# Optimization experiments

Measured on AMD Instinct MI355X. Metric: run time of the kernel, lower is better.

## Reference

```python
import jax, jax.numpy as jnp
import numpy as np

N_NODES = 50000
N_EDGES = 800000
D = 128


def setup_inputs() -> dict:
    key = jax.random.key(0)
    ks = jax.random.split(key, 8)
    scale = 1.0 / np.sqrt(D)
    x = jax.random.normal(ks[0], (N_NODES, D), dtype=jnp.float32)
    edge_index = jax.random.randint(ks[1], (2, N_EDGES), 0, N_NODES, dtype=jnp.int64)
    return {
        "x": x,
        "edge_index": edge_index,
        "w1_l": jax.random.normal(ks[2], (D, D), dtype=jnp.float32) * scale,
        "w1_r": jax.random.normal(ks[3], (D, D), dtype=jnp.float32) * scale,
        "b1": jnp.zeros((D,), dtype=jnp.float32),
        "w2_l": jax.random.normal(ks[4], (D, D), dtype=jnp.float32) * scale,
        "w2_r": jax.random.normal(ks[5], (D, D), dtype=jnp.float32) * scale,
        "b2": jnp.zeros((D,), dtype=jnp.float32),
    }


def _sage_conv(x, src, dst, w_l, w_r, b):
    # mean aggregation of source features at destination nodes
    n = x.shape[0]
    msg = x[src]                                            # [E, D] gather
    agg = jax.ops.segment_sum(msg, dst, num_segments=n)      # [N, D] scatter-add
    cnt = jax.ops.segment_sum(jnp.ones((src.shape[0],), x.dtype), dst, num_segments=n)
    mean = agg / jnp.maximum(cnt, 1.0)[:, None]
    # out = lin_l(mean_agg) + lin_r(x) + bias  (PyG SAGEConv default)
    return mean @ w_l.T + x @ w_r.T + b


def reference(x, edge_index, w1_l, w1_r, b1, w2_l, w2_r, b2):
    src, dst = edge_index[0], edge_index[1]
    h = jax.nn.relu(_sage_conv(x, src, dst, w1_l, w1_r, b1))
    out = _sage_conv(h, src, dst, w2_l, w2_r, b2)
    return out
```

## Files before the change

kernel.cpp:

```cpp
#include <hip/hip_runtime.h>

#define D 128
#define CAP 48
#define TILE 16

typedef unsigned short u16;
typedef unsigned int u32;
typedef _Float16 f16;
typedef __attribute__((ext_vector_type(4))) _Float16 h4;
typedef __attribute__((ext_vector_type(8))) _Float16 h8;
typedef __attribute__((ext_vector_type(4))) float f32x4;

__global__ __launch_bounds__(256) void prep_kernel(const float* __restrict__ x,
                                                   f16* __restrict__ xh, int n8,
                                                   const float* __restrict__ w1l,
                                                   const float* __restrict__ w1r,
                                                   const float* __restrict__ w2l,
                                                   const float* __restrict__ w2r,
                                                   f16* __restrict__ wb1,
                                                   f16* __restrict__ wb2,
                                                   int* __restrict__ cnt, int Nceil,
                                                   int cvtBlocks, int wBlocks) {
    const int b = blockIdx.x;
    const int t = threadIdx.x;
    if (b < cvtBlocks) {
        int i = b * 256 + t;
        if (i < n8) {
            float4 v0 = reinterpret_cast<const float4*>(x)[2 * i];
            float4 v1 = reinterpret_cast<const float4*>(x)[2 * i + 1];
            h8 o;
            o[0] = (f16)v0.x; o[1] = (f16)v0.y; o[2] = (f16)v0.z; o[3] = (f16)v0.w;
            o[4] = (f16)v1.x; o[5] = (f16)v1.y; o[6] = (f16)v1.z; o[7] = (f16)v1.w;
            reinterpret_cast<h8*>(xh)[i] = o;
        }
    } else if (b < cvtBlocks + wBlocks) {
        int e = (b - cvtBlocks) * 256 + t;
        int which = e >> 15;
        int i = e & 32767;
        int j = i >> 8, k = i & 255;
        const float* wl = which ? w2l : w1l;
        const float* wr = which ? w2r : w1r;
        f16* wb = which ? wb2 : wb1;
        float v = (k < 128) ? wl[j * 128 + k] : wr[j * 128 + k - 128];
        wb[i] = (f16)v;
    } else {
        int i = (b - cvtBlocks - wBlocks) * 256 + t;
        if (i < Nceil) cnt[i] = 0;
    }
}

__global__ __launch_bounds__(256) void fill_pad_xcd(const int* __restrict__ src,
                                                    const int* __restrict__ dst,
                                                    int* __restrict__ cnt,
                                                    int* __restrict__ edge_pad,
                                                    int E, int bucketDiv, int perChunk) {
    const int b = blockIdx.x & 7;
    const int chunk = blockIdx.x >> 3;
    const int lo = b * bucketDiv;
    const int hi = lo + bucketDiv;
    const int beg = chunk * perChunk;
    const int end = min(E, beg + perChunk);
    for (int base = beg + threadIdx.x * 4; base < end; base += 1024) {
        if (base + 3 < end) {
            int4 d = *reinterpret_cast<const int4*>(dst + base);
            if (d.x >= lo && d.x < hi) { int p = atomicAdd(&cnt[d.x], 1); if (p < CAP) edge_pad[d.x * CAP + p] = src[base + 0]; }
            if (d.y >= lo && d.y < hi) { int p = atomicAdd(&cnt[d.y], 1); if (p < CAP) edge_pad[d.y * CAP + p] = src[base + 1]; }
            if (d.z >= lo && d.z < hi) { int p = atomicAdd(&cnt[d.z], 1); if (p < CAP) edge_pad[d.z * CAP + p] = src[base + 2]; }
            if (d.w >= lo && d.w < hi) { int p = atomicAdd(&cnt[d.w], 1); if (p < CAP) edge_pad[d.w * CAP + p] = src[base + 3]; }
        } else {
            for (int j = 0; j < 4 && base + j < end; ++j) {
                int d = dst[base + j];
                if (d >= lo && d < hi) { int p = atomicAdd(&cnt[d], 1); if (p < CAP) edge_pad[d * CAP + p] = src[base + j]; }
            }
        }
    }
}

template <int RELU, int OUTF16>
__global__ __launch_bounds__(256) void sage_fused(const f16* __restrict__ feat,
                                                  const int* __restrict__ cnt,
                                                  const int* __restrict__ edge_pad,
                                                  const f16* __restrict__ wb,
                                                  const float* __restrict__ bias,
                                                  float* __restrict__ outf,
                                                  f16* __restrict__ outh, int n) {
    __shared__ f16 sM[TILE * 128];
    __shared__ int eLds[TILE * CAP];
    __shared__ int degLds[TILE];
    const int t = threadIdx.x;
    const int base = blockIdx.x * TILE;
    char* sMb = reinterpret_cast<char*>(sM);

    {
        const int4* gseg = reinterpret_cast<const int4*>(edge_pad + (size_t)base * CAP);
        if (t < TILE * CAP / 4) reinterpret_cast<int4*>(eLds)[t] = gseg[t];
        if (t < TILE) degLds[t] = (base + t < n) ? cnt[base + t] : 0;
    }
    __syncthreads();

    {
        const int halfId = t >> 5;
        const int lane = t & 31;
#pragma unroll
        for (int rnd = 0; rnd < TILE / 8; ++rnd) {
            const int nl = rnd * 8 + halfId;
            const int deg = degLds[nl];
            const int stored = min(deg, CAP);
            const int* ep = &eLds[nl * CAP];

            h4 acc = (h4){0, 0, 0, 0};
            int j = 0;
            for (; j + 16 <= stored; j += 16) {
                int4 i0 = *reinterpret_cast<const int4*>(ep + j);
                int4 i1 = *reinterpret_cast<const int4*>(ep + j + 4);
                int4 i2 = *reinterpret_cast<const int4*>(ep + j + 8);
                int4 i3 = *reinterpret_cast<const int4*>(ep + j + 12);
                h4 v0 = *reinterpret_cast<const h4*>(feat + (size_t)i0.x * D + lane * 4);
                h4 v1 = *reinterpret_cast<const h4*>(feat + (size_t)i0.y * D + lane * 4);
                h4 v2 = *reinterpret_cast<const h4*>(feat + (size_t)i0.z * D + lane * 4);
                h4 v3 = *reinterpret_cast<const h4*>(feat + (size_t)i0.w * D + lane * 4);
                h4 v4 = *reinterpret_cast<const h4*>(feat + (size_t)i1.x * D + lane * 4);
                h4 v5 = *reinterpret_cast<const h4*>(feat + (size_t)i1.y * D + lane * 4);
                h4 v6 = *reinterpret_cast<const h4*>(feat + (size_t)i1.z * D + lane * 4);
                h4 v7 = *reinterpret_cast<const h4*>(feat + (size_t)i1.w * D + lane * 4);
                h4 v8 = *reinterpret_cast<const h4*>(feat + (size_t)i2.x * D + lane * 4);
                h4 v9 = *reinterpret_cast<const h4*>(feat + (size_t)i2.y * D + lane * 4);
                h4 va = *reinterpret_cast<const h4*>(feat + (size_t)i2.z * D + lane * 4);
                h4 vb = *reinterpret_cast<const h4*>(feat + (size_t)i2.w * D + lane * 4);
                h4 vc = *reinterpret_cast<const h4*>(feat + (size_t)i3.x * D + lane * 4);
                h4 vd = *reinterpret_cast<const h4*>(feat + (size_t)i3.y * D + lane * 4);
                h4 ve = *reinterpret_cast<const h4*>(feat + (size_t)i3.z * D + lane * 4);
                h4 vf = *reinterpret_cast<const h4*>(feat + (size_t)i3.w * D + lane * 4);
                acc += ((v0 + v1) + (v2 + v3)) + ((v4 + v5) + (v6 + v7))
                     + ((v8 + v9) + (va + vb)) + ((vc + vd) + (ve + vf));
            }
            for (; j + 4 <= stored; j += 4) {
                int4 ia = *reinterpret_cast<const int4*>(ep + j);
                h4 v0 = *reinterpret_cast<const h4*>(feat + (size_t)ia.x * D + lane * 4);
                h4 v1 = *reinterpret_cast<const h4*>(feat + (size_t)ia.y * D + lane * 4);
                h4 v2 = *reinterpret_cast<const h4*>(feat + (size_t)ia.z * D + lane * 4);
                h4 v3 = *reinterpret_cast<const h4*>(feat + (size_t)ia.w * D + lane * 4);
                acc += (v0 + v1) + (v2 + v3);
            }
            for (; j < stored; ++j) {
                int s = ep[j];
                acc += *reinterpret_cast<const h4*>(feat + (size_t)s * D + lane * 4);
            }

            const f16 sc = (deg > 0) ? (f16)(1.f / (float)deg) : (f16)0;
            h4 o = acc * (h4){sc, sc, sc, sc};
            int lin = nl * 256 + lane * 8;
            *reinterpret_cast<h4*>(sMb + (lin ^ ((nl & 7) << 4))) = o;
        }
    }
    __syncthreads();

    const int wid = t >> 6, lane = t & 63;
    const int l15 = lane & 15, l4 = lane >> 4;
    const int colBase = wid * 32;

    int rowA = base + l15;
    if (rowA >= n) rowA = 0;

    f32x4 acc0 = (f32x4){0.f, 0.f, 0.f, 0.f};
    f32x4 acc1 = (f32x4){0.f, 0.f, 0.f, 0.f};

    const int swr = (l15 & 7) << 4;

#pragma unroll
    for (int ks = 0; ks < 8; ++ks) {
        h8 afr;
        if (ks < 4) {
            int lin = l15 * 256 + ks * 64 + l4 * 16;
            afr = *reinterpret_cast<const h8*>(sMb + (lin ^ swr));
        } else {
            const int kk = (ks & 3) * 32 + l4 * 8;
            afr = *reinterpret_cast<const h8*>(feat + (size_t)rowA * D + kk);
        }
#pragma unroll
        for (int q = 0; q < 2; ++q) {
            h8 bfr = *reinterpret_cast<const h8*>(
                wb + (size_t)(colBase + q * 16 + l15) * 256 + ks * 32 + l4 * 8);
            f32x4& a = q ? acc1 : acc0;
            a = __builtin_amdgcn_mfma_f32_16x16x32_f16(afr, bfr, a, 0, 0, 0);
        }
    }

#pragma unroll
    for (int q = 0; q < 2; ++q) {
        const int col = colBase + q * 16 + l15;
        const float bv = bias[col];
        const f32x4& a = q ? acc1 : acc0;
#pragma unroll
        for (int r = 0; r < 4; ++r) {
            int orow = base + l4 * 4 + r;
            if (orow < n) {
                float v = a[r] + bv;
                if (RELU) v = fmaxf(v, 0.f);
                if (OUTF16)
                    outh[(size_t)orow * D + col] = (f16)v;
                else
                    outf[(size_t)orow * D + col] = v;
            }
        }
    }
}

extern "C" void kernel_launch(void* const* d_in, const int* in_sizes, int n_in,
                              void* d_out, int out_size, void* d_ws, size_t ws_size,
                              hipStream_t stream) {
    const float* x   = (const float*)d_in[0];
    const int*   ei  = (const int*)d_in[1];
    const float* w1l = (const float*)d_in[2];
    const float* w1r = (const float*)d_in[3];
    const float* b1  = (const float*)d_in[4];
    const float* w2l = (const float*)d_in[5];
    const float* w2r = (const float*)d_in[6];
    const float* b2  = (const float*)d_in[7];
    float* out = (float*)d_out;

    const int N = in_sizes[0] / D;
    const int E = in_sizes[1] / 2;

    const int* src = ei;
    const int* dst = ei + E;

    const int gridFused = (N + TILE - 1) / TILE;
    const int Nceil = gridFused * TILE;

    char* ws = (char*)d_ws;
    auto align = [](size_t v) { return (v + 255) & ~(size_t)255; };
    const size_t featB = align((size_t)N * D * sizeof(f16));

    f16* xh       = (f16*)ws;   ws += featB;
    f16* hh       = (f16*)ws;   ws += featB;
    f16* wb1      = (f16*)ws;   ws += align(128 * 256 * sizeof(f16));
    f16* wb2      = (f16*)ws;   ws += align(128 * 256 * sizeof(f16));
    int* cnt      = (int*)ws;   ws += align((size_t)Nceil * sizeof(int));
    int* edge_pad = (int*)ws;   ws += align((size_t)Nceil * CAP * sizeof(int));

    const int n8        = N * D / 8;
    const int cvtBlocks = (n8 + 255) / 256;
    const int wBlocks   = 256;
    const int zBlocks   = (Nceil + 255) / 256;
    const int bucketDiv = (N + 7) / 8;
    const int perChunk  = 5120;
    const int chunks    = (E + perChunk - 1) / perChunk;

    prep_kernel<<<cvtBlocks + wBlocks + zBlocks, 256, 0, stream>>>(
        x, xh, n8, w1l, w1r, w2l, w2r, wb1, wb2, cnt, Nceil, cvtBlocks, wBlocks);

    fill_pad_xcd<<<8 * chunks, 256, 0, stream>>>(src, dst, cnt, edge_pad, E, bucketDiv, perChunk);

    sage_fused<1, 1><<<gridFused, 256, 0, stream>>>(xh, cnt, edge_pad, wb1, b1, nullptr, hh, N);

    sage_fused<0, 0><<<gridFused, 256, 0, stream>>>(hh, cnt, edge_pad, wb2, b2, out, nullptr, N);
}
```

Baseline: 170.3 us.

## Merge edge bucketing into prep kernel and double fused tile rows

```diff
diff --git a/kernel.cpp b/kernel.cpp
--- a/kernel.cpp
+++ b/kernel.cpp
@@ -2,7 +2,7 @@
 
 #define D 128
 #define CAP 48
-#define TILE 16
+#define TILE 32
 
 typedef unsigned short u16;
 typedef unsigned int u32;
@@ -11,16 +11,20 @@
 typedef __attribute__((ext_vector_type(8))) _Float16 h8;
 typedef __attribute__((ext_vector_type(4))) float f32x4;
 
-__global__ __launch_bounds__(256) void prep_kernel(const float* __restrict__ x,
-                                                   f16* __restrict__ xh, int n8,
-                                                   const float* __restrict__ w1l,
-                                                   const float* __restrict__ w1r,
-                                                   const float* __restrict__ w2l,
-                                                   const float* __restrict__ w2r,
-                                                   f16* __restrict__ wb1,
-                                                   f16* __restrict__ wb2,
-                                                   int* __restrict__ cnt, int Nceil,
-                                                   int cvtBlocks, int wBlocks) {
+__global__ __launch_bounds__(256) void mega_prep(const float* __restrict__ x,
+                                                 f16* __restrict__ xh, int n8,
+                                                 const float* __restrict__ w1l,
+                                                 const float* __restrict__ w1r,
+                                                 const float* __restrict__ w2l,
+                                                 const float* __restrict__ w2r,
+                                                 f16* __restrict__ wb1,
+                                                 f16* __restrict__ wb2,
+                                                 const int* __restrict__ src,
+                                                 const int* __restrict__ dst,
+                                                 int* __restrict__ cnt,
+                                                 int* __restrict__ edge_pad,
+                                                 int E, int bucketDiv, int perChunk,
+                                                 int cvtBlocks, int wBlocks) {
     const int b = blockIdx.x;
     const int t = threadIdx.x;
     if (b < cvtBlocks) {
@@ -44,33 +48,25 @@
         float v = (k < 128) ? wl[j * 128 + k] : wr[j * 128 + k - 128];
         wb[i] = (f16)v;
     } else {
-        int i = (b - cvtBlocks - wBlocks) * 256 + t;
-        if (i < Nceil) cnt[i] = 0;
-    }
-}
-
-__global__ __launch_bounds__(256) void fill_pad_xcd(const int* __restrict__ src,
-                                                    const int* __restrict__ dst,
-                                                    int* __restrict__ cnt,
-                                                    int* __restrict__ edge_pad,
-                                                    int E, int bucketDiv, int perChunk) {
-    const int b = blockIdx.x & 7;
-    const int chunk = blockIdx.x >> 3;
-    const int lo = b * bucketDiv;
-    const int hi = lo + bucketDiv;
-    const int beg = chunk * perChunk;
-    const int end = min(E, beg + perChunk);
-    for (int base = beg + threadIdx.x * 4; base < end; base += 1024) {
-        if (base + 3 < end) {
-            int4 d = *reinterpret_cast<const int4*>(dst + base);
-            if (d.x >= lo && d.x < hi) { int p = atomicAdd(&cnt[d.x], 1); if (p < CAP) edge_pad[d.x * CAP + p] = src[base + 0]; }
-            if (d.y >= lo && d.y < hi) { int p = atomicAdd(&cnt[d.y], 1); if (p < CAP) edge_pad[d.y * CAP + p] = src[base + 1]; }
-            if (d.z >= lo && d.z < hi) { int p = atomicAdd(&cnt[d.z], 1); if (p < CAP) edge_pad[d.z * CAP + p] = src[base + 2]; }
-            if (d.w >= lo && d.w < hi) { int p = atomicAdd(&cnt[d.w], 1); if (p < CAP) edge_pad[d.w * CAP + p] = src[base + 3]; }
-        } else {
-            for (int j = 0; j < 4 && base + j < end; ++j) {
-                int d = dst[base + j];
-                if (d >= lo && d < hi) { int p = atomicAdd(&cnt[d], 1); if (p < CAP) edge_pad[d * CAP + p] = src[base + j]; }
+        const int fillIdx = b - cvtBlocks - wBlocks;
+        const int bucket = b & 7;
+        const int chunk = fillIdx >> 3;
+        const int lo = bucket * bucketDiv;
+        const int hi = lo + bucketDiv;
+        const int beg = chunk * perChunk;
+        const int end = min(E, beg + perChunk);
+        for (int base = beg + t * 4; base < end; base += 1024) {
+            if (base + 3 < end) {
+                int4 d = *reinterpret_cast<const int4*>(dst + base);
+                if (d.x >= lo && d.x < hi) { int p = atomicAdd(&cnt[d.x], 1); if (p < CAP) edge_pad[d.x * CAP + p] = src[base + 0]; }
+                if (d.y >= lo && d.y < hi) { int p = atomicAdd(&cnt[d.y], 1); if (p < CAP) edge_pad[d.y * CAP + p] = src[base + 1]; }
+                if (d.z >= lo && d.z < hi) { int p = atomicAdd(&cnt[d.z], 1); if (p < CAP) edge_pad[d.z * CAP + p] = src[base + 2]; }
+                if (d.w >= lo && d.w < hi) { int p = atomicAdd(&cnt[d.w], 1); if (p < CAP) edge_pad[d.w * CAP + p] = src[base + 3]; }
+            } else {
+                for (int j = 0; j < 4 && base + j < end; ++j) {
+                    int d = dst[base + j];
+                    if (d >= lo && d < hi) { int p = atomicAdd(&cnt[d], 1); if (p < CAP) edge_pad[d * CAP + p] = src[base + j]; }
+                }
             }
         }
     }
@@ -93,7 +89,11 @@
 
     {
         const int4* gseg = reinterpret_cast<const int4*>(edge_pad + (size_t)base * CAP);
-        if (t < TILE * CAP / 4) reinterpret_cast<int4*>(eLds)[t] = gseg[t];
+#pragma unroll
+        for (int i = 0; i < (TILE * CAP / 4 + 255) / 256; ++i) {
+            int idx = i * 256 + t;
+            if (idx < TILE * CAP / 4) reinterpret_cast<int4*>(eLds)[idx] = gseg[idx];
+        }
         if (t < TILE) degLds[t] = (base + t < n) ? cnt[base + t] : 0;
     }
     __syncthreads();
@@ -110,29 +110,18 @@
 
             h4 acc = (h4){0, 0, 0, 0};
             int j = 0;
-            for (; j + 16 <= stored; j += 16) {
-                int4 i0 = *reinterpret_cast<const int4*>(ep + j);
-                int4 i1 = *reinterpret_cast<const int4*>(ep + j + 4);
-                int4 i2 = *reinterpret_cast<const int4*>(ep + j + 8);
-                int4 i3 = *reinterpret_cast<const int4*>(ep + j + 12);
-                h4 v0 = *reinterpret_cast<const h4*>(feat + (size_t)i0.x * D + lane * 4);
-                h4 v1 = *reinterpret_cast<const h4*>(feat + (size_t)i0.y * D + lane * 4);
-                h4 v2 = *reinterpret_cast<const h4*>(feat + (size_t)i0.z * D + lane * 4);
-                h4 v3 = *reinterpret_cast<const h4*>(feat + (size_t)i0.w * D + lane * 4);
-                h4 v4 = *reinterpret_cast<const h4*>(feat + (size_t)i1.x * D + lane * 4);
-                h4 v5 = *reinterpret_cast<const h4*>(feat + (size_t)i1.y * D + lane * 4);
-                h4 v6 = *reinterpret_cast<const h4*>(feat + (size_t)i1.z * D + lane * 4);
-                h4 v7 = *reinterpret_cast<const h4*>(feat + (size_t)i1.w * D + lane * 4);
-                h4 v8 = *reinterpret_cast<const h4*>(feat + (size_t)i2.x * D + lane * 4);
-                h4 v9 = *reinterpret_cast<const h4*>(feat + (size_t)i2.y * D + lane * 4);
-                h4 va = *reinterpret_cast<const h4*>(feat + (size_t)i2.z * D + lane * 4);
-                h4 vb = *reinterpret_cast<const h4*>(feat + (size_t)i2.w * D + lane * 4);
-                h4 vc = *reinterpret_cast<const h4*>(feat + (size_t)i3.x * D + lane * 4);
-                h4 vd = *reinterpret_cast<const h4*>(feat + (size_t)i3.y * D + lane * 4);
-                h4 ve = *reinterpret_cast<const h4*>(feat + (size_t)i3.z * D + lane * 4);
-                h4 vf = *reinterpret_cast<const h4*>(feat + (size_t)i3.w * D + lane * 4);
-                acc += ((v0 + v1) + (v2 + v3)) + ((v4 + v5) + (v6 + v7))
-                     + ((v8 + v9) + (va + vb)) + ((vc + vd) + (ve + vf));
+            for (; j + 8 <= stored; j += 8) {
+                int4 ia = *reinterpret_cast<const int4*>(ep + j);
+                int4 ib = *reinterpret_cast<const int4*>(ep + j + 4);
+                h4 v0 = *reinterpret_cast<const h4*>(feat + (size_t)ia.x * D + lane * 4);
+                h4 v1 = *reinterpret_cast<const h4*>(feat + (size_t)ia.y * D + lane * 4);
+                h4 v2 = *reinterpret_cast<const h4*>(feat + (size_t)ia.z * D + lane * 4);
+                h4 v3 = *reinterpret_cast<const h4*>(feat + (size_t)ia.w * D + lane * 4);
+                h4 v4 = *reinterpret_cast<const h4*>(feat + (size_t)ib.x * D + lane * 4);
+                h4 v5 = *reinterpret_cast<const h4*>(feat + (size_t)ib.y * D + lane * 4);
+                h4 v6 = *reinterpret_cast<const h4*>(feat + (size_t)ib.z * D + lane * 4);
+                h4 v7 = *reinterpret_cast<const h4*>(feat + (size_t)ib.w * D + lane * 4);
+                acc += ((v0 + v1) + (v2 + v3)) + ((v4 + v5) + (v6 + v7));
             }
             for (; j + 4 <= stored; j += 4) {
                 int4 ia = *reinterpret_cast<const int4*>(ep + j);
@@ -159,30 +148,43 @@
     const int l15 = lane & 15, l4 = lane >> 4;
     const int colBase = wid * 32;
 
-    int rowA = base + l15;
-    if (rowA >= n) rowA = 0;
-
-    f32x4 acc0 = (f32x4){0.f, 0.f, 0.f, 0.f};
-    f32x4 acc1 = (f32x4){0.f, 0.f, 0.f, 0.f};
+    int rowA[2];
+#pragma unroll
+    for (int m = 0; m < 2; ++m) {
+        int r = base + m * 16 + l15;
+        rowA[m] = (r < n) ? r : 0;
+    }
+
+    f32x4 acc2[2][2];
+#pragma unroll
+    for (int m = 0; m < 2; ++m)
+#pragma unroll
+        for (int q = 0; q < 2; ++q) acc2[m][q] = (f32x4){0.f, 0.f, 0.f, 0.f};
 
     const int swr = (l15 & 7) << 4;
 
 #pragma unroll
     for (int ks = 0; ks < 8; ++ks) {
-        h8 afr;
+        h8 afr[2];
         if (ks < 4) {
-            int lin = l15 * 256 + ks * 64 + l4 * 16;
-            afr = *reinterpret_cast<const h8*>(sMb + (lin ^ swr));
+#pragma unroll
+            for (int m = 0; m < 2; ++m) {
+                int lin = (m * 16 + l15) * 256 + ks * 64 + l4 * 16;
+                afr[m] = *reinterpret_cast<const h8*>(sMb + (lin ^ swr));
+            }
         } else {
             const int kk = (ks & 3) * 32 + l4 * 8;
-            afr = *reinterpret_cast<const h8*>(feat + (size_t)rowA * D + kk);
+#pragma unroll
+            for (int m = 0; m < 2; ++m)
+                afr[m] = *reinterpret_cast<const h8*>(feat + (size_t)rowA[m] * D + kk);
         }
 #pragma unroll
         for (int q = 0; q < 2; ++q) {
             h8 bfr = *reinterpret_cast<const h8*>(
                 wb + (size_t)(colBase + q * 16 + l15) * 256 + ks * 32 + l4 * 8);
-            f32x4& a = q ? acc1 : acc0;
-            a = __builtin_amdgcn_mfma_f32_16x16x32_f16(afr, bfr, a, 0, 0, 0);
+#pragma unroll
+            for (int m = 0; m < 2; ++m)
+                acc2[m][q] = __builtin_amdgcn_mfma_f32_16x16x32_f16(afr[m], bfr, acc2[m][q], 0, 0, 0);
         }
     }
 
@@ -190,17 +192,19 @@
     for (int q = 0; q < 2; ++q) {
         const int col = colBase + q * 16 + l15;
         const float bv = bias[col];
-        const f32x4& a = q ? acc1 : acc0;
-#pragma unroll
-        for (int r = 0; r < 4; ++r) {
-            int orow = base + l4 * 4 + r;
-            if (orow < n) {
-                float v = a[r] + bv;
-                if (RELU) v = fmaxf(v, 0.f);
-                if (OUTF16)
-                    outh[(size_t)orow * D + col] = (f16)v;
-                else
-                    outf[(size_t)orow * D + col] = v;
+#pragma unroll
+        for (int m = 0; m < 2; ++m) {
+#pragma unroll
+            for (int r = 0; r < 4; ++r) {
+                int orow = base + m * 16 + l4 * 4 + r;
+                if (orow < n) {
+                    float v = acc2[m][q][r] + bv;
+                    if (RELU) v = fmaxf(v, 0.f);
+                    if (OUTF16)
+                        outh[(size_t)orow * D + col] = (f16)v;
+                    else
+                        outf[(size_t)orow * D + col] = v;
+                }
             }
         }
     }
@@ -242,15 +246,15 @@
     const int n8        = N * D / 8;
     const int cvtBlocks = (n8 + 255) / 256;
     const int wBlocks   = 256;
-    const int zBlocks   = (Nceil + 255) / 256;
     const int bucketDiv = (N + 7) / 8;
     const int perChunk  = 5120;
     const int chunks    = (E + perChunk - 1) / perChunk;
-
-    prep_kernel<<<cvtBlocks + wBlocks + zBlocks, 256, 0, stream>>>(
-        x, xh, n8, w1l, w1r, w2l, w2r, wb1, wb2, cnt, Nceil, cvtBlocks, wBlocks);
-
-    fill_pad_xcd<<<8 * chunks, 256, 0, stream>>>(src, dst, cnt, edge_pad, E, bucketDiv, perChunk);
+    const int fillBlocks = 8 * chunks;
+
+    hipMemsetAsync(cnt, 0, (size_t)Nceil * sizeof(int), stream);
+    mega_prep<<<cvtBlocks + wBlocks + fillBlocks, 256, 0, stream>>>(
+        x, xh, n8, w1l, w1r, w2l, w2r, wb1, wb2,
+        src, dst, cnt, edge_pad, E, bucketDiv, perChunk, cvtBlocks, wBlocks);
 
     sage_fused<1, 1><<<gridFused, 256, 0, stream>>>(xh, cnt, edge_pad, wb1, b1, nullptr, hh, N);
 
```

New measurement: 152.6 us. 10.4% less time.
